# Kernel tuning notes

Hardware: AMD Instinct MI355X
Metric: run time of the kernel (lower is better)

Reference implementation:

```python
import jax, jax.numpy as jnp
import numpy as np

B, N, C = 4, 1024, 1024
H = 16
D = C // H
FF = 4 * C
EPS = 1e-5


def setup_inputs() -> dict:
    key = jax.random.key(0)
    ks = jax.random.split(key, 16)
    s = 0.02
    return {
        "x": jax.random.normal(ks[0], (B, N, C), jnp.float32),
        "c": jax.random.normal(ks[1], (B, C), jnp.float32),
        "node_mask": jax.random.randint(ks[2], (B, N), 0, 2) > 0,
        "qkv_w": jax.random.normal(ks[3], (C, 3 * C), jnp.float32) * s,
        "proj_w": jax.random.normal(ks[4], (C, C), jnp.float32) * s,
        "proj_b": jnp.zeros((C,), jnp.float32),
        "fc1_w": jax.random.normal(ks[5], (C, FF), jnp.float32) * s,
        "fc1_b": jnp.zeros((FF,), jnp.float32),
        "fc2_w": jax.random.normal(ks[6], (FF, C), jnp.float32) * s,
        "fc2_b": jnp.zeros((C,), jnp.float32),
        "ada1_w": jax.random.normal(ks[7], (C, C), jnp.float32) * s,
        "ada1_b": jnp.zeros((C,), jnp.float32),
        "ada2_w": jax.random.normal(ks[8], (C, 6 * C), jnp.float32) * s,
        "ada2_b": jnp.zeros((6 * C,), jnp.float32),
    }


def _layernorm(x):
    # LayerNorm without affine params (elementwise_affine=False), eps=1e-5
    mu = jnp.mean(x, axis=-1, keepdims=True)
    var = jnp.mean(jnp.square(x - mu), axis=-1, keepdims=True)
    return (x - mu) * jax.lax.rsqrt(var + EPS)


def _modulate(x, shift, scale):
    return x * (1.0 + scale[:, None, :]) + shift[:, None, :]


def _attention(x, node_mask, qkv_w, proj_w, proj_b):
    b, n, c = x.shape
    qkv = (x @ qkv_w).reshape(b, n, 3, H, D)
    q, k, v = jnp.moveaxis(qkv, 2, 0)          # each [b, n, H, D]
    q = q.transpose(0, 2, 1, 3)                # [b, H, n, D]
    k = k.transpose(0, 2, 1, 3)
    v = v.transpose(0, 2, 1, 3)
    scale = D ** -0.5
    scores = jnp.einsum("bhnd,bhmd->bhnm", q, k) * scale
    mask = node_mask[:, None, None, :]          # key mask [b,1,1,n]
    scores = jnp.where(mask, scores, -jnp.inf)
    attn = jax.nn.softmax(scores, axis=-1)
    out = jnp.einsum("bhnm,bhmd->bhnd", attn, v)
    out = out.transpose(0, 2, 1, 3).reshape(b, n, c)
    return out @ proj_w + proj_b


def _mlp(x, fc1_w, fc1_b, fc2_w, fc2_b):
    h = jax.nn.gelu(x @ fc1_w + fc1_b, approximate=False)
    return h @ fc2_w + fc2_b


def reference(x, c, node_mask, qkv_w, proj_w, proj_b, fc1_w, fc1_b,
              fc2_w, fc2_b, ada1_w, ada1_b, ada2_w, ada2_b):
    # adaLN: Linear -> SiLU -> Linear -> 6 chunks along feature dim
    ada = jax.nn.silu(c @ ada1_w + ada1_b) @ ada2_w + ada2_b
    (shift_msa, scale_msa, gate_msa,
     shift_mlp, scale_mlp, gate_mlp) = jnp.split(ada, 6, axis=1)

    attn_out = _attention(x, node_mask, qkv_w, proj_w, proj_b)
    x = x + gate_msa[:, None, :] * _modulate(_layernorm(attn_out), shift_msa, scale_msa)

    mlp_out = _mlp(x, fc1_w, fc1_b, fc2_w, fc2_b)
    x = x + gate_mlp[:, None, :] * _modulate(_layernorm(mlp_out), shift_mlp, scale_mlp)
    return x
```

## Files before the change

### kernel.cpp

```cpp
#include <hip/hip_runtime.h>

typedef unsigned short u16;
typedef __attribute__((ext_vector_type(8))) short short8;
typedef __attribute__((ext_vector_type(8))) unsigned short u16x8;
typedef __attribute__((ext_vector_type(4))) unsigned short u16x4;
typedef __attribute__((ext_vector_type(4))) float f32x4;

#define DEVINL __device__ __forceinline__
#define SGB0 __builtin_amdgcn_sched_barrier(0)

DEVINL u16 f2b(float f) {
    union { float f; unsigned u; } a; a.f = f;
    unsigned r = a.u + 0x7FFFu + ((a.u >> 16) & 1u);
    return (u16)(r >> 16);
}
DEVINL float b2f(u16 h) {
    union { unsigned u; float f; } a; a.u = ((unsigned)h) << 16;
    return a.f;
}

DEVINL void gload16(const void* g, void* l) {
    __builtin_amdgcn_global_load_lds(
        (const __attribute__((address_space(1))) void*)g,
        (__attribute__((address_space(3))) void*)l, 16, 0, 0);
}

__global__ void detect_mask(const unsigned char* __restrict__ m, int nbytes, int* __restrict__ flag) {
    __shared__ int any;
    if (threadIdx.x == 0) any = 0;
    __syncthreads();
    int loc = 0;
    for (int i = threadIdx.x; i < nbytes; i += 256)
        if ((i & 3) && m[i]) loc = 1;
    if (loc) atomicOr(&any, 1);
    __syncthreads();
    if (threadIdx.x == 0) *flag = any;
}

__global__ __launch_bounds__(256) void f32_to_bf16(const float* __restrict__ in, u16* __restrict__ out, int n4) {
    int i = blockIdx.x * 256 + threadIdx.x;
    if (i >= n4) return;
    float4 v = ((const float4*)in)[i];
    u16x4 o = { f2b(v.x), f2b(v.y), f2b(v.z), f2b(v.w) };
    *(u16x4*)(out + (size_t)i * 4) = o;
}

__global__ __launch_bounds__(256) void transpose_bf16(const float* __restrict__ W, u16* __restrict__ WT, int K, int N) {
    __shared__ float tile[32][33];
    int tx = threadIdx.x, ty = threadIdx.y;
    int n0 = blockIdx.x * 32, k0 = blockIdx.y * 32;
#pragma unroll
    for (int i = 0; i < 4; i++)
        tile[ty + i * 8][tx] = W[(size_t)(k0 + ty + i * 8) * N + n0 + tx];
    __syncthreads();
#pragma unroll
    for (int i = 0; i < 4; i++)
        WT[(size_t)(n0 + ty + i * 8) * K + k0 + tx] = f2b(tile[tx][ty + i * 8]);
}

__global__ __launch_bounds__(256) void transpose_v(const u16* __restrict__ qkv, u16* __restrict__ vtg) {
    __shared__ u16 tile[64][72];
    const int bh = blockIdx.x & 63, nt = blockIdx.x >> 6;
    const int b = bh >> 4, h = bh & 15;
    const int t = threadIdx.x;
    const int r = t >> 3, c = (t & 7) << 3;
#pragma unroll
    for (int i = 0; i < 2; i++) {
        int rr = r + i * 32;
        *(u16x8*)&tile[rr][c] =
            *(const u16x8*)&qkv[(size_t)(b * 1024 + nt * 64 + rr) * 3072 + 2048 + h * 64 + c];
    }
    __syncthreads();
#pragma unroll
    for (int i = 0; i < 2; i++) {
        int d = r + i * 32;
        u16x8 o;
#pragma unroll
        for (int e = 0; e < 8; e++) o[e] = tile[c + e][d];
        *(u16x8*)&vtg[(size_t)bh * 65536 + (size_t)d * 1024 + nt * 64 + c] = o;
    }
}

template <int KRLOG2>
__global__ __launch_bounds__(256) void gemv_partial(
    const float* __restrict__ h, const float* __restrict__ w,
    float* __restrict__ part, int N, int K) {
    constexpr int KR = 1 << KRLOG2;
    constexpr int KR4 = KR >> 2;
    __shared__ float hs[4 * KR];
    __shared__ float red[256 * 16];
    const int t = threadIdx.x, wv = t >> 6, l = t & 63;
    const int j4 = blockIdx.x * 256 + l * 4;
    const int kb = blockIdx.y << KRLOG2;
    for (int idx = t; idx < 4 * KR; idx += 256) {
        int b = idx >> KRLOG2, kk = idx & (KR - 1);
        hs[idx] = h[b * K + kb + kk];
    }
    __syncthreads();
    float acc[4][4];
#pragma unroll
    for (int b = 0; b < 4; b++)
#pragma unroll
        for (int c = 0; c < 4; c++) acc[b][c] = 0.f;
    const float* wp = w + (size_t)(kb + wv * KR4) * N + j4;
#pragma unroll
    for (int i = 0; i < KR4; i++) {
        float4 wf = *(const float4*)(wp + (size_t)i * N);
        int kk = wv * KR4 + i;
#pragma unroll
        for (int b = 0; b < 4; b++) {
            float hv = hs[(b << KRLOG2) + kk];
            acc[b][0] += hv * wf.x;
            acc[b][1] += hv * wf.y;
            acc[b][2] += hv * wf.z;
            acc[b][3] += hv * wf.w;
        }
    }
#pragma unroll
    for (int b = 0; b < 4; b++)
#pragma unroll
        for (int c = 0; c < 4; c++)
            red[t * 16 + b * 4 + c] = acc[b][c];
    __syncthreads();
    if (t < 64) {
#pragma unroll
        for (int b = 0; b < 4; b++) {
            float4 s;
            s.x = red[l * 16 + b * 4 + 0] + red[(l + 64) * 16 + b * 4 + 0] + red[(l + 128) * 16 + b * 4 + 0] + red[(l + 192) * 16 + b * 4 + 0];
            s.y = red[l * 16 + b * 4 + 1] + red[(l + 64) * 16 + b * 4 + 1] + red[(l + 128) * 16 + b * 4 + 1] + red[(l + 192) * 16 + b * 4 + 1];
            s.z = red[l * 16 + b * 4 + 2] + red[(l + 64) * 16 + b * 4 + 2] + red[(l + 128) * 16 + b * 4 + 2] + red[(l + 192) * 16 + b * 4 + 2];
            s.w = red[l * 16 + b * 4 + 3] + red[(l + 64) * 16 + b * 4 + 3] + red[(l + 128) * 16 + b * 4 + 3] + red[(l + 192) * 16 + b * 4 + 3];
            *(float4*)&part[(size_t)(blockIdx.y * 4 + b) * N + j4] = s;
        }
    }
}

template <int SILU>
__global__ __launch_bounds__(256) void gemv_reduce(
    const float* __restrict__ part, const float* __restrict__ bias,
    float* __restrict__ out, int N, int NK) {
    int gid = blockIdx.x * 256 + threadIdx.x;
    int b = gid / N, j = gid - b * N;
    float s = bias[j];
    for (int i = 0; i < NK; i++) s += part[(size_t)(i * 4 + b) * N + j];
    if (SILU) s = s / (1.f + __expf(-s));
    out[gid] = s;
}

template <int EPI>
__global__ __launch_bounds__(512) void gemm256(
    const u16* __restrict__ A, const u16* __restrict__ B, const float* __restrict__ bias,
    u16* __restrict__ Cb, u16* __restrict__ Cb2, int M, int N, int lda, int Ksub) {
    __shared__ u16 As[2][256 * 64];
    __shared__ u16 Bs[2][256 * 64];
    const int t = threadIdx.x;
    const int w = t >> 6, l = t & 63;
    const int l15 = l & 15, lg = l >> 4;
    const int nTN = N >> 8;
    const int ntiles = (M >> 8) * nTN;
    const int sk = blockIdx.x / ntiles;
    int tb = blockIdx.x - sk * ntiles;
    tb = (tb & 7) * (ntiles >> 3) + (tb >> 3);
    const int tm = tb / nTN, tn = tb - tm * nTN;
    const int row0 = tm << 8, col0 = tn << 8;
    const int wr = (w >> 2) << 7, wc = (w & 3) << 6;
    const int k_begin = sk * Ksub;

    const int rA = t >> 3;
    const int cswz = ((t & 7) ^ (rA & 7)) << 3;
    const u16* gA = A + (size_t)(row0 + rA) * lda + cswz + k_begin;
    const u16* gB = B + (size_t)(col0 + rA) * lda + cswz + k_begin;
    const int rsw = l15 & 7;

    f32x4 acc[8][4];
#pragma unroll
    for (int i = 0; i < 8; i++)
#pragma unroll
        for (int j = 0; j < 4; j++) acc[i][j] = (f32x4){0.f, 0.f, 0.f, 0.f};

    const int nkt = Ksub >> 6;

    auto STAGE = [&](int kt, int s) {
        const int k0 = kt << 6;
#pragma unroll
        for (int j = 0; j < 4; j++)
            gload16(gA + (size_t)j * 64 * lda + k0, As[s] + j * 4096 + w * 512);
#pragma unroll
        for (int j = 0; j < 4; j++)
            gload16(gB + (size_t)j * 64 * lda + k0, Bs[s] + j * 4096 + w * 512);
    };

    STAGE(0, 0);
    STAGE(1, 1);
    asm volatile("s_waitcnt vmcnt(8)" ::: "memory");
    SGB0;
    __builtin_amdgcn_s_barrier();
    SGB0;

    for (int it = 0; it < nkt; ++it) {
        const int cur = it & 1;
        short8 af0[8], bf0[4];
        {
            const int chunk = (lg ^ rsw) << 3;
#pragma unroll
            for (int mi = 0; mi < 8; mi++)
                af0[mi] = *(const short8*)&As[cur][((wr + mi * 16 + l15) << 6) + chunk];
#pragma unroll
            for (int ni = 0; ni < 4; ni++)
                bf0[ni] = *(const short8*)&Bs[cur][((wc + ni * 16 + l15) << 6) + chunk];
        }
        __builtin_amdgcn_s_setprio(1);
#pragma unroll
        for (int mi = 0; mi < 8; mi++)
#pragma unroll
            for (int ni = 0; ni < 4; ni++)
                acc[mi][ni] = __builtin_amdgcn_mfma_f32_16x16x32_bf16(af0[mi], bf0[ni], acc[mi][ni], 0, 0, 0);
        __builtin_amdgcn_s_setprio(0);
        short8 af1[8], bf1[4];
        {
            const int chunk = ((4 + lg) ^ rsw) << 3;
#pragma unroll
            for (int mi = 0; mi < 8; mi++)
                af1[mi] = *(const short8*)&As[cur][((wr + mi * 16 + l15) << 6) + chunk];
#pragma unroll
            for (int ni = 0; ni < 4; ni++)
                bf1[ni] = *(const short8*)&Bs[cur][((wc + ni * 16 + l15) << 6) + chunk];
        }
        asm volatile("s_waitcnt lgkmcnt(0)" ::: "memory");
        SGB0;
        __builtin_amdgcn_s_barrier();
        SGB0;
        if (it + 2 < nkt) STAGE(it + 2, cur);
        __builtin_amdgcn_s_setprio(1);
#pragma unroll
        for (int mi = 0; mi < 8; mi++)
#pragma unroll
            for (int ni = 0; ni < 4; ni++)
                acc[mi][ni] = __builtin_amdgcn_mfma_f32_16x16x32_bf16(af1[mi], bf1[ni], acc[mi][ni], 0, 0, 0);
        __builtin_amdgcn_s_setprio(0);
        if (it + 1 < nkt) {
            if (it + 2 < nkt) asm volatile("s_waitcnt vmcnt(8)" ::: "memory");
            else              asm volatile("s_waitcnt vmcnt(0)" ::: "memory");
            SGB0;
            __builtin_amdgcn_s_barrier();
            SGB0;
        }
    }

    const size_t MNsz = (size_t)M * N;
    u16* dst = (sk < 2) ? Cb + (size_t)sk * MNsz : Cb2 + (size_t)(sk - 2) * MNsz;
#pragma unroll
    for (int mi = 0; mi < 8; mi++) {
#pragma unroll
        for (int ni = 0; ni < 4; ni++) {
#pragma unroll
            for (int j = 0; j < 4; j++) {
                int r = row0 + wr + mi * 16 + (lg << 2) + j;
                int c = col0 + wc + ni * 16 + l15;
                float v = acc[mi][ni][j];
                if (EPI == 0) {
                    dst[(size_t)r * N + c] = f2b(v);
                } else {
                    float vv = v + bias[c];
                    float g = 0.5f * vv * (1.f + erff(vv * 0.70710678118f));
                    dst[(size_t)r * N + c] = f2b(g);
                }
            }
        }
    }
}

__global__ __launch_bounds__(256) void attn_kernel(
    const u16* __restrict__ qkv, const u16* __restrict__ vtg,
    const unsigned char* __restrict__ maskb,
    const int* __restrict__ flagp, u16* __restrict__ out) {
    __shared__ u16 Qs[64 * 64];
    __shared__ u16 Ks[64 * 64];
    __shared__ u16 Vt[64 * 64];
    __shared__ u16 Ps[64 * 64];
    __shared__ float maskf[64];
    __shared__ float alpha_lds[64];
    __shared__ float lst_lds[64];

    int bi = (int)blockIdx.x;
    bi = (bi & 7) * 128 + (bi >> 3);
    const int qt = bi & 15, h = (bi >> 4) & 15, b = bi >> 8;
    const int t = threadIdx.x, w = t >> 6, l = t & 63;
    const int l15 = l & 15, lg = l >> 4;
    const int rsw = l15 & 7;
    const int flag = *flagp;
    const int q0 = qt << 6;
    const int bh = b * 16 + h;

    const int sr = t >> 3, sc = t & 7;
#pragma unroll
    for (int i = 0; i < 2; i++) {
        int r = sr + i * 32;
        u16x8 v = *(const u16x8*)&qkv[(size_t)(b * 1024 + q0 + r) * 3072 + h * 64 + sc * 8];
        u16x8 o;
#pragma unroll
        for (int e = 0; e < 8; e++) o[e] = f2b(b2f(v[e]) * 0.125f);
        *(u16x8*)&Qs[r * 64 + ((sc ^ (r & 7)) << 3)] = o;
    }

    f32x4 O[4];
#pragma unroll
    for (int nd = 0; nd < 4; nd++) O[nd] = (f32x4){0.f, 0.f, 0.f, 0.f};
    float mst = -1e30f, lst = 0.f;

    u16x8 kreg[2], vreg[2];
    float mnext;
    {
#pragma unroll
        for (int i = 0; i < 2; i++) {
            kreg[i] = *(const u16x8*)&qkv[(size_t)(b * 1024 + sr + i * 32) * 3072 + h * 64 + 1024 + sc * 8];
            vreg[i] = *(const u16x8*)&vtg[(size_t)bh * 65536 + (size_t)(sr + i * 32) * 1024 + sc * 8];
        }
        int gi = b * 1024 + (t & 63);
        bool ms = flag ? (maskb[gi] != 0) : (((const int*)maskb)[gi] != 0);
        mnext = ms ? 1.f : 0.f;
    }

    for (int kt = 0; kt < 16; kt++) {
        __syncthreads();
#pragma unroll
        for (int i = 0; i < 2; i++) {
            int r = sr + i * 32;
            *(u16x8*)&Ks[r * 64 + ((sc ^ (r & 7)) << 3)] = kreg[i];
            *(u16x8*)&Vt[r * 64 + ((sc ^ (r & 7)) << 3)] = vreg[i];
        }
        if (t < 64) maskf[t] = mnext;
        __syncthreads();
        if (kt < 15) {
            const int kn = (kt + 1) << 6;
#pragma unroll
            for (int i = 0; i < 2; i++) {
                kreg[i] = *(const u16x8*)&qkv[(size_t)(b * 1024 + kn + sr + i * 32) * 3072 + h * 64 + 1024 + sc * 8];
                vreg[i] = *(const u16x8*)&vtg[(size_t)bh * 65536 + (size_t)(sr + i * 32) * 1024 + kn + sc * 8];
            }
            int gi = b * 1024 + kn + (t & 63);
            bool ms = flag ? (maskb[gi] != 0) : (((const int*)maskb)[gi] != 0);
            mnext = ms ? 1.f : 0.f;
        }

        f32x4 S[4];
#pragma unroll
        for (int mi = 0; mi < 4; mi++) S[mi] = (f32x4){0.f, 0.f, 0.f, 0.f};
        __builtin_amdgcn_s_setprio(1);
#pragma unroll
        for (int ks = 0; ks < 2; ks++) {
            const int chunk = (((ks << 2) + lg) ^ rsw) << 3;
            short8 bq = *(const short8*)&Qs[(w * 16 + l15) * 64 + chunk];
#pragma unroll
            for (int mi = 0; mi < 4; mi++) {
                short8 ak = *(const short8*)&Ks[(mi * 16 + l15) * 64 + chunk];
                S[mi] = __builtin_amdgcn_mfma_f32_16x16x32_bf16(ak, bq, S[mi], 0, 0, 0);
            }
        }
        __builtin_amdgcn_s_setprio(0);

        float pm = -1e30f;
#pragma unroll
        for (int mi = 0; mi < 4; mi++) {
            f32x4 mk = *(const f32x4*)&maskf[mi * 16 + (lg << 2)];
#pragma unroll
            for (int j = 0; j < 4; j++) {
                float xv = (mk[j] > 0.f) ? S[mi][j] : -1e30f;
                S[mi][j] = xv;
                pm = fmaxf(pm, xv);
            }
        }
        pm = fmaxf(pm, __shfl_xor(pm, 16));
        pm = fmaxf(pm, __shfl_xor(pm, 32));

        bool skip = __all(pm <= mst + 8.f);
        float alpha = 1.f;
        if (!skip) {
            float mn = fmaxf(mst, pm);
            alpha = __expf(mst - mn);
            mst = mn;
        }

        float psum = 0.f;
        const int prow = w * 16 + l15;
#pragma unroll
        for (int mi = 0; mi < 4; mi++) {
            f32x4 mk = *(const f32x4*)&maskf[mi * 16 + (lg << 2)];
            u16x4 v4;
#pragma unroll
            for (int j = 0; j < 4; j++) {
                float p = __expf(S[mi][j] - mst) * mk[j];
                psum += p;
                v4[j] = f2b(p);
            }
            int ch = ((mi * 2 + (lg >> 1)) ^ rsw);
            *(u16x4*)&Ps[prow * 64 + (ch << 3) + ((lg & 1) << 2)] = v4;
        }
        psum += __shfl_xor(psum, 16);
        psum += __shfl_xor(psum, 32);
        lst = lst * alpha + psum;

        if (!skip) {
            if (lg == 0) alpha_lds[w * 16 + l15] = alpha;
            f32x4 af = *(const f32x4*)&alpha_lds[w * 16 + (lg << 2)];
#pragma unroll
            for (int nd = 0; nd < 4; nd++)
#pragma unroll
                for (int j = 0; j < 4; j++) O[nd][j] *= af[j];
        }

        __builtin_amdgcn_s_setprio(1);
#pragma unroll
        for (int ks = 0; ks < 2; ks++) {
            const int chunk = (((ks << 2) + lg) ^ rsw) << 3;
            short8 pa = *(const short8*)&Ps[(w * 16 + l15) * 64 + chunk];
#pragma unroll
            for (int nd = 0; nd < 4; nd++) {
                short8 bv = *(const short8*)&Vt[(nd * 16 + l15) * 64 + chunk];
                O[nd] = __builtin_amdgcn_mfma_f32_16x16x32_bf16(pa, bv, O[nd], 0, 0, 0);
            }
        }
        __builtin_amdgcn_s_setprio(0);
    }

    if (lg == 0) lst_lds[w * 16 + l15] = lst;
    f32x4 lf = *(const f32x4*)&lst_lds[w * 16 + (lg << 2)];
#pragma unroll
    for (int nd = 0; nd < 4; nd++)
#pragma unroll
        for (int j = 0; j < 4; j++) {
            int r = b * 1024 + q0 + w * 16 + (lg << 2) + j;
            int c = h * 64 + nd * 16 + l15;
            out[(size_t)r * 1024 + c] = f2b(O[nd][j] / lf[j]);
        }
}

__global__ __launch_bounds__(256) void ln_mod_res4(
    const u16* __restrict__ s0, const u16* __restrict__ s1, const float* __restrict__ bias,
    const float* __restrict__ resid, const float* __restrict__ ada, int oS, int oC, int oG,
    float* __restrict__ outf, u16* __restrict__ outb) {
    __shared__ float red[8];
    const int row = blockIdx.x, t = threadIdx.x, b = row >> 10;
    const float4 bv = ((const float4*)bias)[t];
    const size_t MN = 1ull << 22;
    const u16* p0 = s0 + (size_t)row * 1024 + t * 4;
    const u16* p1 = s1 + (size_t)row * 1024 + t * 4;
    u16x4 a0 = *(const u16x4*)p0;
    u16x4 a1 = *(const u16x4*)(p0 + MN);
    u16x4 a2 = *(const u16x4*)p1;
    u16x4 a3 = *(const u16x4*)(p1 + MN);
    float4 v;
    v.x = (b2f(a0[0]) + b2f(a1[0])) + (b2f(a2[0]) + b2f(a3[0])) + bv.x;
    v.y = (b2f(a0[1]) + b2f(a1[1])) + (b2f(a2[1]) + b2f(a3[1])) + bv.y;
    v.z = (b2f(a0[2]) + b2f(a1[2])) + (b2f(a2[2]) + b2f(a3[2])) + bv.z;
    v.w = (b2f(a0[3]) + b2f(a1[3])) + (b2f(a2[3]) + b2f(a3[3])) + bv.w;
    float s = v.x + v.y + v.z + v.w;
    float q = v.x * v.x + v.y * v.y + v.z * v.z + v.w * v.w;
#pragma unroll
    for (int off = 32; off >= 1; off >>= 1) {
        s += __shfl_down(s, off);
        q += __shfl_down(q, off);
    }
    if ((t & 63) == 0) { red[(t >> 6) * 2] = s; red[(t >> 6) * 2 + 1] = q; }
    __syncthreads();
    float sum = red[0] + red[2] + red[4] + red[6];
    float sq = red[1] + red[3] + red[5] + red[7];
    float mu = sum * (1.f / 1024.f);
    float var = sq * (1.f / 1024.f) - mu * mu;
    float rinv = rsqrtf(var + 1e-5f);
    const float* ad = ada + b * 6144;
    const float4 rv = ((const float4*)(resid + (size_t)row * 1024))[t];
    const float4 sc = ((const float4*)(ad + oC))[t];
    const float4 sh = ((const float4*)(ad + oS))[t];
    const float4 gt = ((const float4*)(ad + oG))[t];
    float4 o;
    o.x = rv.x + gt.x * ((v.x - mu) * rinv * (1.f + sc.x) + sh.x);
    o.y = rv.y + gt.y * ((v.y - mu) * rinv * (1.f + sc.y) + sh.y);
    o.z = rv.z + gt.z * ((v.z - mu) * rinv * (1.f + sc.z) + sh.z);
    o.w = rv.w + gt.w * ((v.w - mu) * rinv * (1.f + sc.w) + sh.w);
    ((float4*)(outf + (size_t)row * 1024))[t] = o;
    if (outb) {
        u16x4 ob = { f2b(o.x), f2b(o.y), f2b(o.z), f2b(o.w) };
        *(u16x4*)(outb + (size_t)row * 1024 + t * 4) = ob;
    }
}

extern "C" void kernel_launch(void* const* d_in, const int* in_sizes, int n_in,
                              void* d_out, int out_size, void* d_ws, size_t ws_size,
                              hipStream_t stream) {
    (void)in_sizes; (void)n_in; (void)out_size; (void)ws_size;
    const float* x = (const float*)d_in[0];
    const float* cvec = (const float*)d_in[1];
    const unsigned char* maskb = (const unsigned char*)d_in[2];
    const float* qkv_w = (const float*)d_in[3];
    const float* proj_w = (const float*)d_in[4];
    const float* proj_b = (const float*)d_in[5];
    const float* fc1_w = (const float*)d_in[6];
    const float* fc1_b = (const float*)d_in[7];
    const float* fc2_w = (const float*)d_in[8];
    const float* fc2_b = (const float*)d_in[9];
    const float* ada1_w = (const float*)d_in[10];
    const float* ada1_b = (const float*)d_in[11];
    const float* ada2_w = (const float*)d_in[12];
    const float* ada2_b = (const float*)d_in[13];
    float* outp = (float*)d_out;

    char* ws = (char*)d_ws;
    size_t off = 0;
    auto nxt = [&](size_t bytes) { size_t r = off; off += (bytes + 255) & ~(size_t)255; return r; };
    u16* qkvwT  = (u16*)(ws + nxt(3072ull * 1024 * 2));
    u16* projwT = (u16*)(ws + nxt(1024ull * 1024 * 2));
    u16* fc1wT  = (u16*)(ws + nxt(4096ull * 1024 * 2));
    u16* fc2wT  = (u16*)(ws + nxt(1024ull * 4096 * 2));
    float* adah = (float*)(ws + nxt(4ull * 1024 * 4));
    float* ada  = (float*)(ws + nxt(4ull * 6144 * 4));
    float* part1 = (float*)(ws + nxt(32ull * 4 * 1024 * 4));
    float* part2 = (float*)(ws + nxt(8ull * 4 * 6144 * 4));
    int* flag   = (int*)(ws + nxt(256));
    u16* xbf = (u16*)(ws + nxt(4096ull * 1024 * 2));
    u16* attn_buf = xbf;
    char* regC = ws + nxt(2ull * 4096 * 1024 * 4);
    u16* qkvbf = (u16*)regC;
    u16* projpart = (u16*)regC;
    u16* hbuf = (u16*)regC;
    float* y1 = (float*)(ws + nxt(4096ull * 1024 * 4));
    u16* y1b = (u16*)(ws + nxt(4096ull * 1024 * 2));
    u16* fc2part = (u16*)(ws + nxt(2ull * 4096 * 1024 * 2));
    u16* vtg = fc2part;
    u16* fc2partB = (u16*)ws;
    const size_t MN = 4096ull * 1024;

    detect_mask<<<1, 256, 0, stream>>>(maskb, 4096, flag);
    f32_to_bf16<<<4096, 256, 0, stream>>>(x, xbf, 1048576);
    transpose_bf16<<<dim3(96, 32), dim3(32, 8), 0, stream>>>(qkv_w, qkvwT, 1024, 3072);
    transpose_bf16<<<dim3(32, 32), dim3(32, 8), 0, stream>>>(proj_w, projwT, 1024, 1024);
    transpose_bf16<<<dim3(128, 32), dim3(32, 8), 0, stream>>>(fc1_w, fc1wT, 1024, 4096);
    transpose_bf16<<<dim3(32, 128), dim3(32, 8), 0, stream>>>(fc2_w, fc2wT, 4096, 1024);

    gemv_partial<5><<<dim3(4, 32), 256, 0, stream>>>(cvec, ada1_w, part1, 1024, 1024);
    gemv_reduce<1><<<16, 256, 0, stream>>>(part1, ada1_b, adah, 1024, 32);
    gemv_partial<7><<<dim3(24, 8), 256, 0, stream>>>(adah, ada2_w, part2, 6144, 1024);
    gemv_reduce<0><<<96, 256, 0, stream>>>(part2, ada2_b, ada, 6144, 8);

    gemm256<0><<<192, 512, 0, stream>>>(xbf, qkvwT, nullptr, qkvbf, nullptr, 4096, 3072, 1024, 1024);
    transpose_v<<<1024, 256, 0, stream>>>(qkvbf, vtg);
    attn_kernel<<<1024, 256, 0, stream>>>(qkvbf, vtg, maskb, flag, attn_buf);
    gemm256<0><<<256, 512, 0, stream>>>(attn_buf, projwT, nullptr, projpart, projpart + 2 * MN,
                                        4096, 1024, 1024, 256);
    ln_mod_res4<<<4096, 256, 0, stream>>>(projpart, projpart + 2 * MN, proj_b,
                                          x, ada, 0, 1024, 2048, y1, y1b);
    gemm256<2><<<256, 512, 0, stream>>>(y1b, fc1wT, fc1_b, hbuf, nullptr, 4096, 4096, 1024, 1024);
    gemm256<0><<<256, 512, 0, stream>>>(hbuf, fc2wT, nullptr, fc2part, fc2partB, 4096, 1024, 4096, 1024);
    ln_mod_res4<<<4096, 256, 0, stream>>>(fc2part, fc2partB, fc2_b,
                                          y1, ada, 3072, 4096, 5120, outp, nullptr);
}
```

Before: 264.7 us.

## Split GEMM main loop into four quadrant phases with interleaved global staging

Restructures the 256x256 bf16 GEMM inner loop so each k-tile is processed as four accumulator quadrants, each with its own LDS fragment loads, barrier and MFMA burst. Global-to-LDS loads for tile k+2 are issued in pieces between quadrants, as soon as each piece of the buffer is no longer being read. The aim is to overlap memory traffic with MFMA work at a finer grain and lower register pressure from fragment arrays. In exchange it adds four barriers per k-tile instead of two and relies on carefully tuned vmcnt counts.

```diff
diff --git a/kernel.cpp b/kernel.cpp
--- a/kernel.cpp
+++ b/kernel.cpp
@@ -180,71 +180,113 @@
 
     const int nkt = Ksub >> 6;
 
-    auto STAGE = [&](int kt, int s) {
-        const int k0 = kt << 6;
-#pragma unroll
-        for (int j = 0; j < 4; j++)
-            gload16(gA + (size_t)j * 64 * lda + k0, As[s] + j * 4096 + w * 512);
-#pragma unroll
-        for (int j = 0; j < 4; j++)
-            gload16(gB + (size_t)j * 64 * lda + k0, Bs[s] + j * 4096 + w * 512);
+    auto SA = [&](int kt, int j) {
+        gload16(gA + (size_t)j * 64 * lda + (kt << 6), As[kt & 1] + j * 4096 + w * 512);
     };
-
-    STAGE(0, 0);
-    STAGE(1, 1);
-    asm volatile("s_waitcnt vmcnt(8)" ::: "memory");
-    SGB0;
-    __builtin_amdgcn_s_barrier();
-    SGB0;
-
-    for (int it = 0; it < nkt; ++it) {
-        const int cur = it & 1;
-        short8 af0[8], bf0[4];
-        {
-            const int chunk = (lg ^ rsw) << 3;
-#pragma unroll
-            for (int mi = 0; mi < 8; mi++)
-                af0[mi] = *(const short8*)&As[cur][((wr + mi * 16 + l15) << 6) + chunk];
-#pragma unroll
-            for (int ni = 0; ni < 4; ni++)
-                bf0[ni] = *(const short8*)&Bs[cur][((wc + ni * 16 + l15) << 6) + chunk];
-        }
+    auto SB = [&](int kt, int j) {
+        gload16(gB + (size_t)j * 64 * lda + (kt << 6), Bs[kt & 1] + j * 4096 + w * 512);
+    };
+
+    SA(0, 0); SA(0, 2); SB(0, 0); SB(0, 1); SB(0, 2); SB(0, 3); SA(0, 1); SA(0, 3);
+    SA(1, 0); SA(1, 2); SB(1, 0); SB(1, 1); SB(1, 2); SB(1, 3); SA(1, 1); SA(1, 3);
+
+    for (int kt = 0; kt < nkt; ++kt) {
+        const int cur = kt & 1;
+        const bool last = (kt == nkt - 1);
+        const bool stg = (kt + 2 < nkt);
+
+        if (last) asm volatile("s_waitcnt vmcnt(2)" ::: "memory");
+        else      asm volatile("s_waitcnt vmcnt(10)" ::: "memory");
+        SGB0;
+        __builtin_amdgcn_s_barrier();
+        SGB0;
+        short8 a0[2][4], b0[2][2];
+#pragma unroll
+        for (int ks = 0; ks < 2; ks++) {
+            const int chunk = (((ks << 2) + lg) ^ rsw) << 3;
+#pragma unroll
+            for (int mi = 0; mi < 4; mi++)
+                a0[ks][mi] = *(const short8*)&As[cur][((wr + mi * 16 + l15) << 6) + chunk];
+#pragma unroll
+            for (int ni = 0; ni < 2; ni++)
+                b0[ks][ni] = *(const short8*)&Bs[cur][((wc + ni * 16 + l15) << 6) + chunk];
+        }
+        asm volatile("s_waitcnt lgkmcnt(0)" ::: "memory");
+        SGB0;
         __builtin_amdgcn_s_setprio(1);
 #pragma unroll
-        for (int mi = 0; mi < 8; mi++)
-#pragma unroll
-            for (int ni = 0; ni < 4; ni++)
-                acc[mi][ni] = __builtin_amdgcn_mfma_f32_16x16x32_bf16(af0[mi], bf0[ni], acc[mi][ni], 0, 0, 0);
+        for (int ks = 0; ks < 2; ks++)
+#pragma unroll
+            for (int mi = 0; mi < 4; mi++)
+#pragma unroll
+                for (int ni = 0; ni < 2; ni++)
+                    acc[mi][ni] = __builtin_amdgcn_mfma_f32_16x16x32_bf16(a0[ks][mi], b0[ks][ni], acc[mi][ni], 0, 0, 0);
         __builtin_amdgcn_s_setprio(0);
-        short8 af1[8], bf1[4];
-        {
-            const int chunk = ((4 + lg) ^ rsw) << 3;
-#pragma unroll
-            for (int mi = 0; mi < 8; mi++)
-                af1[mi] = *(const short8*)&As[cur][((wr + mi * 16 + l15) << 6) + chunk];
-#pragma unroll
-            for (int ni = 0; ni < 4; ni++)
-                bf1[ni] = *(const short8*)&Bs[cur][((wc + ni * 16 + l15) << 6) + chunk];
-        }
+
+        SGB0;
+        __builtin_amdgcn_s_barrier();
+        SGB0;
+        short8 b1[2][2];
+#pragma unroll
+        for (int ks = 0; ks < 2; ks++) {
+            const int chunk = (((ks << 2) + lg) ^ rsw) << 3;
+#pragma unroll
+            for (int ni = 0; ni < 2; ni++)
+                b1[ks][ni] = *(const short8*)&Bs[cur][((wc + (ni + 2) * 16 + l15) << 6) + chunk];
+        }
+        if (stg) { SA(kt + 2, 0); SA(kt + 2, 2); }
         asm volatile("s_waitcnt lgkmcnt(0)" ::: "memory");
         SGB0;
+        __builtin_amdgcn_s_setprio(1);
+#pragma unroll
+        for (int ks = 0; ks < 2; ks++)
+#pragma unroll
+            for (int mi = 0; mi < 4; mi++)
+#pragma unroll
+                for (int ni = 0; ni < 2; ni++)
+                    acc[mi][ni + 2] = __builtin_amdgcn_mfma_f32_16x16x32_bf16(a0[ks][mi], b1[ks][ni], acc[mi][ni + 2], 0, 0, 0);
+        __builtin_amdgcn_s_setprio(0);
+
+        if (last)     asm volatile("s_waitcnt vmcnt(0)" ::: "memory");
+        else if (stg) asm volatile("s_waitcnt vmcnt(10)" ::: "memory");
+        else          asm volatile("s_waitcnt vmcnt(8)" ::: "memory");
+        SGB0;
         __builtin_amdgcn_s_barrier();
         SGB0;
-        if (it + 2 < nkt) STAGE(it + 2, cur);
+        short8 a1[2][4];
+#pragma unroll
+        for (int ks = 0; ks < 2; ks++) {
+            const int chunk = (((ks << 2) + lg) ^ rsw) << 3;
+#pragma unroll
+            for (int mi = 0; mi < 4; mi++)
+                a1[ks][mi] = *(const short8*)&As[cur][((wr + (mi + 4) * 16 + l15) << 6) + chunk];
+        }
+        if (stg) { SB(kt + 2, 0); SB(kt + 2, 1); SB(kt + 2, 2); SB(kt + 2, 3); }
+        asm volatile("s_waitcnt lgkmcnt(0)" ::: "memory");
+        SGB0;
         __builtin_amdgcn_s_setprio(1);
 #pragma unroll
-        for (int mi = 0; mi < 8; mi++)
-#pragma unroll
-            for (int ni = 0; ni < 4; ni++)
-                acc[mi][ni] = __builtin_amdgcn_mfma_f32_16x16x32_bf16(af1[mi], bf1[ni], acc[mi][ni], 0, 0, 0);
+        for (int ks = 0; ks < 2; ks++)
+#pragma unroll
+            for (int mi = 0; mi < 4; mi++)
+#pragma unroll
+                for (int ni = 0; ni < 2; ni++)
+                    acc[mi + 4][ni] = __builtin_amdgcn_mfma_f32_16x16x32_bf16(a1[ks][mi], b0[ks][ni], acc[mi + 4][ni], 0, 0, 0);
         __builtin_amdgcn_s_setprio(0);
-        if (it + 1 < nkt) {
-            if (it + 2 < nkt) asm volatile("s_waitcnt vmcnt(8)" ::: "memory");
-            else              asm volatile("s_waitcnt vmcnt(0)" ::: "memory");
-            SGB0;
-            __builtin_amdgcn_s_barrier();
-            SGB0;
-        }
+
+        SGB0;
+        __builtin_amdgcn_s_barrier();
+        SGB0;
+        if (stg) { SA(kt + 2, 1); SA(kt + 2, 3); }
+        __builtin_amdgcn_s_setprio(1);
+#pragma unroll
+        for (int ks = 0; ks < 2; ks++)
+#pragma unroll
+            for (int mi = 0; mi < 4; mi++)
+#pragma unroll
+                for (int ni = 0; ni < 2; ni++)
+                    acc[mi + 4][ni + 2] = __builtin_amdgcn_mfma_f32_16x16x32_bf16(a1[ks][mi], b1[ks][ni], acc[mi + 4][ni + 2], 0, 0, 0);
+        __builtin_amdgcn_s_setprio(0);
     }
 
     const size_t MNsz = (size_t)M * N;
```

Result: no change. 267.9 us (+1.2%).
